# Kernel tuning notes

Hardware: AMD Instinct MI355X
Metric: run time of the kernel (lower is better)

## Reference

```python
import jax, jax.numpy as jnp
import numpy as np

B, L, T = 8, 1024, 10
K = 1.0                 # soft_sign sharpness (config.k)
S = float(np.log(9.0))  # self.s
W_PEN = 1.0             # self.w


def soft_sign(x):
    return jax.nn.sigmoid(2.0 * K * x)


def mlp2(f, W1, b1, W2, b2):
    # pointwise 2-layer MLP with ReLU after each layer; output dim 1 -> squeeze
    h = jax.nn.relu(jnp.einsum('...i,oi->...o', f, W1) + b1)
    return jax.nn.relu(jnp.einsum('...i,oi->...o', h, W2) + b2)[..., 0]


def setup_inputs() -> dict:
    key = jax.random.key(0)
    ks = jax.random.split(key, 16)
    u = jax.random.normal(ks[0], (B, L, L), jnp.float32)
    x = jax.random.uniform(ks[1], (B, L, 4), jnp.float32)
    p = lambda k, s: (jax.random.normal(k, s, jnp.float32) * 0.5)
    return dict(
        u=u, x=x, timesteps=T,
        aW1=p(ks[2], (T, 3, 3)), ab1=p(ks[3], (T, 3)), aW2=p(ks[4], (T, 1, 3)), ab2=p(ks[5], (T, 1)),
        rW1=p(ks[6], (T, 3, 3)), rb1=p(ks[7], (T, 3)), rW2=p(ks[8], (T, 1, 3)), rb2=p(ks[9], (T, 1)),
        lW1=p(ks[10], (T, 3, 2)), lb1=p(ks[11], (T, 3)), lW2=p(ks[12], (T, 1, 3)), lb2=p(ks[13], (T, 1)),
    )


def reference(u, x, timesteps, aW1, ab1, aW2, ab2, rW1, rb1, rW2, rb2, lW1, lb1, lW2, lb2):
    # constraint matrix m: sum of symmetrized outer products of base channels
    ba, bu, bc, bg = x[:, :, 0], x[:, :, 1], x[:, :, 2], x[:, :, 3]
    def sym_outer(p, q):
        o = jnp.einsum('bi,bj->bij', p, q)
        return o + o.swapaxes(-1, -2)
    m = sym_outer(ba, bu) + sym_outer(bc, bg) + sym_outer(bu, bg)

    def contact(ah):
        aa = ah * ah
        return (aa + aa.swapaxes(-1, -2)) * 0.5 * m

    uu = soft_sign(u - S) * u
    a_hat = jax.nn.sigmoid(uu) * soft_sign(uu - S)
    a = contact(a_hat)
    lmbd = W_PEN * jax.nn.relu(jnp.sum(a, -1) - 1.0)

    outs = []
    for t in range(timesteps):  # fixed unroll, distinct params per step
        grad_a = -uu * 0.5 + (lmbd * soft_sign(jnp.sum(a, -1) - 1.0))[..., None]
        grad = a_hat * m * (grad_a + grad_a.swapaxes(-1, -2))
        feats = jnp.stack([a_hat, grad, uu], -1)  # [B,L,L,3]
        ah_new = mlp2(feats, aW1[t], ab1[t], aW2[t], ab2[t])
        rho = mlp2(feats, rW1[t], rb1[t], rW2[t], rb2[t])
        ah_new = jnp.clip(jax.nn.relu(jnp.abs(ah_new) - rho), -1.0, 1.0)
        a = contact(ah_new)
        lg = jax.nn.relu(jnp.sum(a, -1) - 1.0)
        lmbd = mlp2(jnp.stack([lmbd, lg], -1), lW1[t], lb1[t], lW2[t], lb2[t])
        a_hat = ah_new
        outs.append(a)
    return jnp.stack(outs)  # [T,B,L,L] == a_t_list[1:]
```

## Files before the change

### kernel.cpp

```cpp
#include <hip/hip_runtime.h>
#include <hip/hip_bf16.h>

#define BB 8
#define LL 1024
#define TT 10
#define TILE 64
#define NTILE (LL/TILE)
#define NPAIR (NTILE*(NTILE+1)/2)
#define SPAD 65
#define S_CONST 2.1972245773362196f

typedef __hip_bfloat16 bf16;

static __device__ __forceinline__ float sigm(float v) {
    return 1.0f / (1.0f + __expf(-v));
}

static __device__ __forceinline__ unsigned short f2bf(float v) {
    bf16 h = __float2bfloat16(v);
    unsigned short b; __builtin_memcpy(&b, &h, 2); return b;
}
static __device__ __forceinline__ float lo2f(unsigned int v) {
    return __uint_as_float(v << 16);
}
static __device__ __forceinline__ float hi2f(unsigned int v) {
    return __uint_as_float(v & 0xffff0000u);
}
static __device__ __forceinline__ unsigned int pk2(float uu, float ah) {
    return (unsigned int)f2bf(uu) | ((unsigned int)f2bf(ah) << 16);
}
static __device__ __forceinline__ unsigned int pk_rt(float uu_exact, float ah) {
    return (__float_as_uint(uu_exact) >> 16) | ((unsigned int)f2bf(ah) << 16);
}

static __device__ __forceinline__ void pair_from_idx(int p, int& I, int& J) {
    int i = 0;
    while (p >= NTILE - i) { p -= NTILE - i; i++; }
    I = i; J = i + p;
}

static __device__ __forceinline__ float mlp3(float f0, float f1, float f2, const float* w) {
    float h0 = fmaxf(w[0]*f0 + w[1]*f1 + w[2]*f2 + w[9],  0.0f);
    float h1 = fmaxf(w[3]*f0 + w[4]*f1 + w[5]*f2 + w[10], 0.0f);
    float h2 = fmaxf(w[6]*f0 + w[7]*f1 + w[8]*f2 + w[11], 0.0f);
    return fmaxf(w[12]*h0 + w[13]*h1 + w[14]*h2 + w[15], 0.0f);
}

static __device__ __forceinline__ float ahnew_calc(float ah, float grad, float uuv, const float* w) {
    float va = mlp3(ah, grad, uuv, w);
    float vr = mlp3(ah, grad, uuv, w + 16);
    float v = fmaxf(fabsf(va) - vr, 0.0f);
    return fminf(v, 1.0f);
}

__global__ __launch_bounds__(256) void k_init(const float* __restrict__ u,
                                              const float* __restrict__ x,
                                              unsigned int* __restrict__ st,
                                              float* __restrict__ rs0) {
    __shared__ float stA[TILE * SPAD];
    __shared__ float stB[TILE * SPAD];
    __shared__ float xI[4 * TILE], xJ[4 * TILE];
    __shared__ float rsI[TILE], rsJ[TILE];

    int b = blockIdx.x / NPAIR, p = blockIdx.x % NPAIR;
    int I, J; pair_from_idx(p, I, J);
    int Ib = I * TILE, Jb = J * TILE;
    bool diag = (I == J);
    int tid = threadIdx.x, c = tid & 63, rg = tid >> 6;

    { int row = tid >> 2, k2 = tid & 3;
      xI[k2*TILE + row] = x[((size_t)b*LL + Ib + row)*4 + k2];
      xJ[k2*TILE + row] = x[((size_t)b*LL + Jb + row)*4 + k2]; }
    if (tid < TILE) { rsI[tid] = 0.0f; rsJ[tid] = 0.0f; }

    float ahv[16];
    size_t baseIJ = ((size_t)b*LL + Ib)*LL + Jb;
    #pragma unroll
    for (int k = 0; k < 16; k++) {
        size_t idx = baseIJ + (size_t)(rg + 4*k)*LL + c;
        float uv  = u[idx];
        float uuv = sigm(2.0f*(uv - S_CONST)) * uv;
        float ah  = sigm(uuv) * sigm(2.0f*(uuv - S_CONST));
        unsigned int pkd = pk2(uuv, ah);
        st[idx] = pkd;
        ahv[k] = hi2f(pkd);
    }
    size_t baseJI = ((size_t)b*LL + Jb)*LL + Ib;
    #pragma unroll
    for (int k = 0; k < 16; k++) {
        int xr = rg + 4*k;
        size_t idx = baseJI + (size_t)xr*LL + c;
        float uv  = u[idx];
        float uuv = sigm(2.0f*(uv - S_CONST)) * uv;
        float ah  = sigm(uuv) * sigm(2.0f*(uuv - S_CONST));
        unsigned int pkd = pk2(uuv, ah);
        if (!diag) st[idx] = pkd;
        stB[xr*SPAD + c] = hi2f(pkd);
    }
    __syncthreads();

    float buj = xJ[1*TILE + c], bgj = xJ[3*TILE + c];
    float s1j = xJ[0*TILE + c] + bgj;
    float s2j = xJ[2*TILE + c] + buj;
    float rsJ_th = 0.0f;
    #pragma unroll
    for (int k = 0; k < 16; k++) {
        int r = rg + 4*k;
        float ah_ij = ahv[k];
        float ah_ji = stB[c*SPAD + r];
        float m = xI[0*TILE + r]*buj + xI[2*TILE + r]*bgj
                + xI[1*TILE + r]*s1j + xI[3*TILE + r]*s2j;
        float a0 = 0.5f * (ah_ij*ah_ij + ah_ji*ah_ji) * m;
        stA[c*SPAD + r] = a0;
        rsJ_th += a0;
    }
    if (!diag) atomicAdd(&rsJ[c], rsJ_th);
    __syncthreads();
    { int r = tid & 63, g = tid >> 6;
      float s = 0.0f;
      #pragma unroll
      for (int q = 0; q < 16; q++) s += stA[(g*16 + q)*SPAD + r];
      atomicAdd(&rsI[r], s); }
    __syncthreads();
    if (tid < TILE) atomicAdd(&rs0[b*LL + Ib + tid], rsI[tid]);
    else if (!diag && tid < 2*TILE) atomicAdd(&rs0[b*LL + Jb + (tid - TILE)], rsJ[tid - TILE]);
}

__global__ __launch_bounds__(256) void k_step(
        unsigned int* __restrict__ st, const float* __restrict__ x,
        const float* __restrict__ rs_cur, float* __restrict__ rs_next,
        const float* __restrict__ lmbd_prev, float* __restrict__ lmbd_next,
        const float* __restrict__ aW1, const float* __restrict__ ab1,
        const float* __restrict__ aW2, const float* __restrict__ ab2,
        const float* __restrict__ rW1, const float* __restrict__ rb1,
        const float* __restrict__ rW2, const float* __restrict__ rb2,
        const float* __restrict__ lw1, const float* __restrict__ lb1_,
        const float* __restrict__ lw2, const float* __restrict__ lb2_,
        float* __restrict__ out, int t) {
    __shared__ float stA[TILE * SPAD];
    __shared__ float stB[TILE * SPAD];
    __shared__ float xI[4 * TILE], xJ[4 * TILE];
    __shared__ float lsI[TILE], lsJ[TILE];
    __shared__ float w[32];
    __shared__ float rsI[TILE], rsJ[TILE];

    int b = blockIdx.x / NPAIR, p = blockIdx.x % NPAIR;
    int I, J; pair_from_idx(p, I, J);
    int Ib = I * TILE, Jb = J * TILE;
    bool diag = (I == J);
    int tid = threadIdx.x, c = tid & 63, rg = tid >> 6;

    float uuv[16], ahv[16];
    size_t baseIJ = ((size_t)b*LL + Ib)*LL + Jb;
    #pragma unroll
    for (int k = 0; k < 16; k++) {
        unsigned int v = st[baseIJ + (size_t)(rg + 4*k)*LL + c];
        uuv[k] = lo2f(v);
        ahv[k] = hi2f(v);
    }

    if (tid < 32) {
        float v;
        if      (tid <  9) v = aW1[t*9 + tid];
        else if (tid < 12) v = ab1[t*3 + (tid-9)];
        else if (tid < 15) v = aW2[t*3 + (tid-12)];
        else if (tid < 16) v = ab2[t];
        else if (tid < 25) v = rW1[t*9 + (tid-16)];
        else if (tid < 28) v = rb1[t*3 + (tid-25)];
        else if (tid < 31) v = rW2[t*3 + (tid-28)];
        else               v = rb2[t];
        w[tid] = v;
    }
    { int row = tid >> 2, k2 = tid & 3;
      xI[k2*TILE + row] = x[((size_t)b*LL + Ib + row)*4 + k2];
      xJ[k2*TILE + row] = x[((size_t)b*LL + Jb + row)*4 + k2]; }
    if (tid < TILE) { rsI[tid] = 0.0f; rsJ[tid] = 0.0f; }
    if (tid < 128) {
        int row = (tid < 64) ? (Ib + tid) : (Jb + tid - 64);
        float rsv = rs_cur[b*LL + row];
        float lg  = fmaxf(rsv - 1.0f, 0.0f);
        float lam;
        if (t == 0) {
            lam = lg;
        } else {
            float l0 = lmbd_prev[b*LL + row];
            float h0 = fmaxf(lw1[0]*l0 + lw1[1]*lg + lb1_[0], 0.0f);
            float h1 = fmaxf(lw1[2]*l0 + lw1[3]*lg + lb1_[1], 0.0f);
            float h2 = fmaxf(lw1[4]*l0 + lw1[5]*lg + lb1_[2], 0.0f);
            lam = fmaxf(lw2[0]*h0 + lw2[1]*h1 + lw2[2]*h2 + lb2_[0], 0.0f);
        }
        float lsv = lam * sigm(2.0f*(rsv - 1.0f));
        if (tid < 64) {
            lsI[tid] = lsv;
            if (diag) lmbd_next[b*LL + row] = lam;
        } else {
            lsJ[tid - 64] = lsv;
        }
    }
    size_t baseJI = ((size_t)b*LL + Jb)*LL + Ib;
    #pragma unroll
    for (int k = 0; k < 16; k++) {
        int xr = rg + 4*k;
        unsigned int v = st[baseJI + (size_t)xr*LL + c];
        stA[xr*SPAD + c] = lo2f(v);
        stB[xr*SPAD + c] = hi2f(v);
    }
    __syncthreads();

    float buj = xJ[1*TILE + c], bgj = xJ[3*TILE + c];
    float s1j = xJ[0*TILE + c] + bgj;
    float s2j = xJ[2*TILE + c] + buj;
    size_t outBase = (((size_t)t*BB + b) * LL) * LL;
    float rsJ_th = 0.0f;
    #pragma unroll
    for (int k = 0; k < 16; k++) {
        int r = rg + 4*k;
        size_t idxIJ = baseIJ + (size_t)r*LL + c;
        float uu_ij = uuv[k];
        float ah_ij = ahv[k];
        float uu_ji = stA[c*SPAD + r];
        float ah_ji = stB[c*SPAD + r];
        float m = xI[0*TILE + r]*buj + xI[2*TILE + r]*bgj
                + xI[1*TILE + r]*s1j + xI[3*TILE + r]*s2j;
        float gsum = -0.5f * (uu_ij + uu_ji) + lsI[r] + lsJ[c];
        float an_ij = ahnew_calc(ah_ij, ah_ij * m * gsum, uu_ij, w);
        float an_ji = ahnew_calc(ah_ji, ah_ji * m * gsum, uu_ji, w);
        float a_val = 0.5f * (an_ij*an_ij + an_ji*an_ji) * m;

        st[idxIJ] = pk_rt(uu_ij, an_ij);
        __builtin_nontemporal_store(a_val, &out[outBase + (size_t)(Ib + r)*LL + (Jb + c)]);

        stA[c*SPAD + r] = a_val;
        stB[c*SPAD + r] = __uint_as_float(pk_rt(uu_ji, an_ji));
        rsJ_th += a_val;
    }
    if (!diag) atomicAdd(&rsJ[c], rsJ_th);
    __syncthreads();
    if (!diag) {
        #pragma unroll
        for (int k = 0; k < 16; k++) {
            int xr = rg + 4*k;
            st[baseJI + (size_t)xr*LL + c] = __float_as_uint(stB[xr*SPAD + c]);
            __builtin_nontemporal_store(stA[xr*SPAD + c],
                                        &out[outBase + (size_t)(Jb + xr)*LL + (Ib + c)]);
        }
    }
    if (t != TT-1) {
        int r = tid & 63, g = tid >> 6;
        float s = 0.0f;
        #pragma unroll
        for (int q = 0; q < 16; q++) s += stA[(g*16 + q)*SPAD + r];
        atomicAdd(&rsI[r], s);
        __syncthreads();
        if (tid < TILE) atomicAdd(&rs_next[b*LL + Ib + tid], rsI[tid]);
        else if (!diag && tid < 2*TILE) atomicAdd(&rs_next[b*LL + Jb + (tid - TILE)], rsJ[tid - TILE]);
    }
}

extern "C" void kernel_launch(void* const* d_in, const int* in_sizes, int n_in,
                              void* d_out, int out_size, void* d_ws, size_t ws_size,
                              hipStream_t stream) {
    const float* u   = (const float*)d_in[0];
    const float* x   = (const float*)d_in[1];
    const float* aW1 = (const float*)d_in[3];
    const float* ab1 = (const float*)d_in[4];
    const float* aW2 = (const float*)d_in[5];
    const float* ab2 = (const float*)d_in[6];
    const float* rW1 = (const float*)d_in[7];
    const float* rb1 = (const float*)d_in[8];
    const float* rW2 = (const float*)d_in[9];
    const float* rb2 = (const float*)d_in[10];
    const float* lW1 = (const float*)d_in[11];
    const float* lb1 = (const float*)d_in[12];
    const float* lW2 = (const float*)d_in[13];
    const float* lb2 = (const float*)d_in[14];
    float* out = (float*)d_out;

    char* ws = (char*)d_ws;
    size_t stBytes = (size_t)BB * LL * LL * sizeof(unsigned int);
    unsigned int* st = (unsigned int*)ws;
    float* rs    = (float*)(ws + stBytes);
    float* lmbdA = rs + (size_t)TT * BB * LL;
    float* lmbdB = lmbdA + BB * LL;

    hipMemsetAsync(rs, 0, (size_t)TT * BB * LL * sizeof(float), stream);
    hipLaunchKernelGGL(k_init, dim3(BB*NPAIR), dim3(256), 0, stream, u, x, st, rs);

    for (int t = 0; t < TT; ++t) {
        float* lnext = (t & 1) ? lmbdB : lmbdA;
        float* lprev = (t & 1) ? lmbdA : lmbdB;
        const float* rs_cur = rs + (size_t)t * BB * LL;
        float* rs_nextp = (t < TT-1) ? (rs + (size_t)(t+1) * BB * LL) : rs;
        int toff = (t > 0) ? (t - 1) : 0;
        hipLaunchKernelGGL(k_step, dim3(BB*NPAIR), dim3(256), 0, stream,
                           st, x, rs_cur, rs_nextp, lprev, lnext,
                           aW1, ab1, aW2, ab2, rW1, rb1, rW2, rb2,
                           lW1 + toff*6, lb1 + toff*3, lW2 + toff*3, lb2 + toff,
                           out, t);
    }
}
```

Measured before the change: 591.2 us.

## Fuse all timesteps into one persistent kernel with LDS-resident state and grid barriers

```diff
diff --git a/kernel.cpp b/kernel.cpp
--- a/kernel.cpp
+++ b/kernel.cpp
@@ -5,9 +5,9 @@
 #define LL 1024
 #define TT 10
 #define TILE 64
-#define NTILE (LL/TILE)
-#define NPAIR (NTILE*(NTILE+1)/2)
-#define SPAD 65
+#define NTILE 16
+#define NOFF 120
+#define NBLK 1024
 #define S_CONST 2.1972245773362196f
 
 typedef __hip_bfloat16 bf16;
@@ -15,28 +15,27 @@
 static __device__ __forceinline__ float sigm(float v) {
     return 1.0f / (1.0f + __expf(-v));
 }
-
 static __device__ __forceinline__ unsigned short f2bf(float v) {
     bf16 h = __float2bfloat16(v);
     unsigned short b; __builtin_memcpy(&b, &h, 2); return b;
 }
-static __device__ __forceinline__ float lo2f(unsigned int v) {
-    return __uint_as_float(v << 16);
-}
-static __device__ __forceinline__ float hi2f(unsigned int v) {
-    return __uint_as_float(v & 0xffff0000u);
-}
+static __device__ __forceinline__ float lo2f(unsigned int v) { return __uint_as_float(v << 16); }
+static __device__ __forceinline__ float hi2f(unsigned int v) { return __uint_as_float(v & 0xffff0000u); }
 static __device__ __forceinline__ unsigned int pk2(float uu, float ah) {
     return (unsigned int)f2bf(uu) | ((unsigned int)f2bf(ah) << 16);
 }
-static __device__ __forceinline__ unsigned int pk_rt(float uu_exact, float ah) {
-    return (__float_as_uint(uu_exact) >> 16) | ((unsigned int)f2bf(ah) << 16);
-}
-
-static __device__ __forceinline__ void pair_from_idx(int p, int& I, int& J) {
-    int i = 0;
-    while (p >= NTILE - i) { p -= NTILE - i; i++; }
-    I = i; J = i + p;
+
+static __device__ __forceinline__ void grid_bar(unsigned int* bar, int slot) {
+    __syncthreads();
+    if (threadIdx.x == 0) {
+        __hip_atomic_fetch_add(&bar[slot], 1u, __ATOMIC_ACQ_REL, __HIP_MEMORY_SCOPE_AGENT);
+        for (int it = 0; it < (1 << 21); ++it) {
+            if (__hip_atomic_load(&bar[slot], __ATOMIC_ACQUIRE, __HIP_MEMORY_SCOPE_AGENT) >= NBLK)
+                break;
+            __builtin_amdgcn_s_sleep(8);
+        }
+    }
+    __syncthreads();
 }
 
 static __device__ __forceinline__ float mlp3(float f0, float f1, float f2, const float* w) {
@@ -45,7 +44,6 @@
     float h2 = fmaxf(w[6]*f0 + w[7]*f1 + w[8]*f2 + w[11], 0.0f);
     return fmaxf(w[12]*h0 + w[13]*h1 + w[14]*h2 + w[15], 0.0f);
 }
-
 static __device__ __forceinline__ float ahnew_calc(float ah, float grad, float uuv, const float* w) {
     float va = mlp3(ah, grad, uuv, w);
     float vr = mlp3(ah, grad, uuv, w + 16);
@@ -53,207 +51,302 @@
     return fminf(v, 1.0f);
 }
 
-__global__ __launch_bounds__(256) void k_init(const float* __restrict__ u,
-                                              const float* __restrict__ x,
-                                              unsigned int* __restrict__ st,
-                                              float* __restrict__ rs0) {
-    __shared__ float stA[TILE * SPAD];
-    __shared__ float stB[TILE * SPAD];
-    __shared__ float xI[4 * TILE], xJ[4 * TILE];
-    __shared__ float rsI[TILE], rsJ[TILE];
-
-    int b = blockIdx.x / NPAIR, p = blockIdx.x % NPAIR;
-    int I, J; pair_from_idx(p, I, J);
-    int Ib = I * TILE, Jb = J * TILE;
-    bool diag = (I == J);
-    int tid = threadIdx.x, c = tid & 63, rg = tid >> 6;
-
-    { int row = tid >> 2, k2 = tid & 3;
-      xI[k2*TILE + row] = x[((size_t)b*LL + Ib + row)*4 + k2];
-      xJ[k2*TILE + row] = x[((size_t)b*LL + Jb + row)*4 + k2]; }
-    if (tid < TILE) { rsI[tid] = 0.0f; rsJ[tid] = 0.0f; }
-
-    float ahv[16];
-    size_t baseIJ = ((size_t)b*LL + Ib)*LL + Jb;
-    #pragma unroll
-    for (int k = 0; k < 16; k++) {
-        size_t idx = baseIJ + (size_t)(rg + 4*k)*LL + c;
-        float uv  = u[idx];
-        float uuv = sigm(2.0f*(uv - S_CONST)) * uv;
-        float ah  = sigm(uuv) * sigm(2.0f*(uuv - S_CONST));
-        unsigned int pkd = pk2(uuv, ah);
-        st[idx] = pkd;
-        ahv[k] = hi2f(pkd);
-    }
-    size_t baseJI = ((size_t)b*LL + Jb)*LL + Ib;
-    #pragma unroll
-    for (int k = 0; k < 16; k++) {
-        int xr = rg + 4*k;
-        size_t idx = baseJI + (size_t)xr*LL + c;
-        float uv  = u[idx];
-        float uuv = sigm(2.0f*(uv - S_CONST)) * uv;
-        float ah  = sigm(uuv) * sigm(2.0f*(uuv - S_CONST));
-        unsigned int pkd = pk2(uuv, ah);
-        if (!diag) st[idx] = pkd;
-        stB[xr*SPAD + c] = hi2f(pkd);
-    }
-    __syncthreads();
-
-    float buj = xJ[1*TILE + c], bgj = xJ[3*TILE + c];
-    float s1j = xJ[0*TILE + c] + bgj;
-    float s2j = xJ[2*TILE + c] + buj;
-    float rsJ_th = 0.0f;
-    #pragma unroll
-    for (int k = 0; k < 16; k++) {
-        int r = rg + 4*k;
-        float ah_ij = ahv[k];
-        float ah_ji = stB[c*SPAD + r];
-        float m = xI[0*TILE + r]*buj + xI[2*TILE + r]*bgj
-                + xI[1*TILE + r]*s1j + xI[3*TILE + r]*s2j;
-        float a0 = 0.5f * (ah_ij*ah_ij + ah_ji*ah_ji) * m;
-        stA[c*SPAD + r] = a0;
-        rsJ_th += a0;
-    }
-    if (!diag) atomicAdd(&rsJ[c], rsJ_th);
-    __syncthreads();
-    { int r = tid & 63, g = tid >> 6;
-      float s = 0.0f;
-      #pragma unroll
-      for (int q = 0; q < 16; q++) s += stA[(g*16 + q)*SPAD + r];
-      atomicAdd(&rsI[r], s); }
-    __syncthreads();
-    if (tid < TILE) atomicAdd(&rs0[b*LL + Ib + tid], rsI[tid]);
-    else if (!diag && tid < 2*TILE) atomicAdd(&rs0[b*LL + Jb + (tid - TILE)], rsJ[tid - TILE]);
-}
-
-__global__ __launch_bounds__(256) void k_step(
-        unsigned int* __restrict__ st, const float* __restrict__ x,
-        const float* __restrict__ rs_cur, float* __restrict__ rs_next,
-        const float* __restrict__ lmbd_prev, float* __restrict__ lmbd_next,
+__global__ __launch_bounds__(256, 4) void k_main(
+        const float* __restrict__ u, const float* __restrict__ x,
+        float* __restrict__ rs, unsigned int* __restrict__ bar,
+        float* __restrict__ out,
         const float* __restrict__ aW1, const float* __restrict__ ab1,
         const float* __restrict__ aW2, const float* __restrict__ ab2,
         const float* __restrict__ rW1, const float* __restrict__ rb1,
         const float* __restrict__ rW2, const float* __restrict__ rb2,
-        const float* __restrict__ lw1, const float* __restrict__ lb1_,
-        const float* __restrict__ lw2, const float* __restrict__ lb2_,
-        float* __restrict__ out, int t) {
-    __shared__ float stA[TILE * SPAD];
-    __shared__ float stB[TILE * SPAD];
-    __shared__ float xI[4 * TILE], xJ[4 * TILE];
+        const float* __restrict__ lW1, const float* __restrict__ lb1,
+        const float* __restrict__ lW2, const float* __restrict__ lb2) {
+    __shared__ unsigned int stA[TILE * 65];
+    __shared__ unsigned int stB[TILE * 65];
+    __shared__ float buf[8 * 65];
+    __shared__ float xIl[4 * TILE];
     __shared__ float lsI[TILE], lsJ[TILE];
+    __shared__ float rsIb[TILE], rsJb[TILE];
     __shared__ float w[32];
-    __shared__ float rsI[TILE], rsJ[TILE];
-
-    int b = blockIdx.x / NPAIR, p = blockIdx.x % NPAIR;
-    int I, J; pair_from_idx(p, I, J);
-    int Ib = I * TILE, Jb = J * TILE;
-    bool diag = (I == J);
-    int tid = threadIdx.x, c = tid & 63, rg = tid >> 6;
-
-    float uuv[16], ahv[16];
-    size_t baseIJ = ((size_t)b*LL + Ib)*LL + Jb;
-    #pragma unroll
-    for (int k = 0; k < 16; k++) {
-        unsigned int v = st[baseIJ + (size_t)(rg + 4*k)*LL + c];
-        uuv[k] = lo2f(v);
-        ahv[k] = hi2f(v);
-    }
-
-    if (tid < 32) {
-        float v;
-        if      (tid <  9) v = aW1[t*9 + tid];
-        else if (tid < 12) v = ab1[t*3 + (tid-9)];
-        else if (tid < 15) v = aW2[t*3 + (tid-12)];
-        else if (tid < 16) v = ab2[t];
-        else if (tid < 25) v = rW1[t*9 + (tid-16)];
-        else if (tid < 28) v = rb1[t*3 + (tid-25)];
-        else if (tid < 31) v = rW2[t*3 + (tid-28)];
-        else               v = rb2[t];
-        w[tid] = v;
-    }
-    { int row = tid >> 2, k2 = tid & 3;
-      xI[k2*TILE + row] = x[((size_t)b*LL + Ib + row)*4 + k2];
-      xJ[k2*TILE + row] = x[((size_t)b*LL + Jb + row)*4 + k2]; }
-    if (tid < TILE) { rsI[tid] = 0.0f; rsJ[tid] = 0.0f; }
-    if (tid < 128) {
-        int row = (tid < 64) ? (Ib + tid) : (Jb + tid - 64);
-        float rsv = rs_cur[b*LL + row];
-        float lg  = fmaxf(rsv - 1.0f, 0.0f);
-        float lam;
-        if (t == 0) {
-            lam = lg;
-        } else {
-            float l0 = lmbd_prev[b*LL + row];
-            float h0 = fmaxf(lw1[0]*l0 + lw1[1]*lg + lb1_[0], 0.0f);
-            float h1 = fmaxf(lw1[2]*l0 + lw1[3]*lg + lb1_[1], 0.0f);
-            float h2 = fmaxf(lw1[4]*l0 + lw1[5]*lg + lb1_[2], 0.0f);
-            lam = fmaxf(lw2[0]*h0 + lw2[1]*h1 + lw2[2]*h2 + lb2_[0], 0.0f);
-        }
-        float lsv = lam * sigm(2.0f*(rsv - 1.0f));
-        if (tid < 64) {
-            lsI[tid] = lsv;
-            if (diag) lmbd_next[b*LL + row] = lam;
-        } else {
-            lsJ[tid - 64] = lsv;
-        }
-    }
-    size_t baseJI = ((size_t)b*LL + Jb)*LL + Ib;
-    #pragma unroll
-    for (int k = 0; k < 16; k++) {
-        int xr = rg + 4*k;
-        unsigned int v = st[baseJI + (size_t)xr*LL + c];
-        stA[xr*SPAD + c] = lo2f(v);
-        stB[xr*SPAD + c] = hi2f(v);
-    }
-    __syncthreads();
-
-    float buj = xJ[1*TILE + c], bgj = xJ[3*TILE + c];
-    float s1j = xJ[0*TILE + c] + bgj;
-    float s2j = xJ[2*TILE + c] + buj;
-    size_t outBase = (((size_t)t*BB + b) * LL) * LL;
-    float rsJ_th = 0.0f;
-    #pragma unroll
-    for (int k = 0; k < 16; k++) {
-        int r = rg + 4*k;
-        size_t idxIJ = baseIJ + (size_t)r*LL + c;
-        float uu_ij = uuv[k];
-        float ah_ij = ahv[k];
-        float uu_ji = stA[c*SPAD + r];
-        float ah_ji = stB[c*SPAD + r];
-        float m = xI[0*TILE + r]*buj + xI[2*TILE + r]*bgj
-                + xI[1*TILE + r]*s1j + xI[3*TILE + r]*s2j;
-        float gsum = -0.5f * (uu_ij + uu_ji) + lsI[r] + lsJ[c];
-        float an_ij = ahnew_calc(ah_ij, ah_ij * m * gsum, uu_ij, w);
-        float an_ji = ahnew_calc(ah_ji, ah_ji * m * gsum, uu_ji, w);
-        float a_val = 0.5f * (an_ij*an_ij + an_ji*an_ji) * m;
-
-        st[idxIJ] = pk_rt(uu_ij, an_ij);
-        __builtin_nontemporal_store(a_val, &out[outBase + (size_t)(Ib + r)*LL + (Jb + c)]);
-
-        stA[c*SPAD + r] = a_val;
-        stB[c*SPAD + r] = __uint_as_float(pk_rt(uu_ji, an_ji));
-        rsJ_th += a_val;
-    }
-    if (!diag) atomicAdd(&rsJ[c], rsJ_th);
-    __syncthreads();
-    if (!diag) {
+
+    int gid = blockIdx.x, tid = threadIdx.x;
+    int c = tid & 63, rg = tid >> 6;
+    float lam = 0.0f;
+
+    if (gid < BB * NOFF) {
+        int b = gid / NOFF, po = gid % NOFF;
+        int i = 0; while (po >= NTILE - 1 - i) { po -= NTILE - 1 - i; i++; }
+        int Ib = i * TILE, Jb = (i + 1 + po) * TILE;
+
+        float xc0 = x[((size_t)b*LL + Jb + c)*4 + 0], xc1 = x[((size_t)b*LL + Jb + c)*4 + 1];
+        float xc2 = x[((size_t)b*LL + Jb + c)*4 + 2], xc3 = x[((size_t)b*LL + Jb + c)*4 + 3];
+        float bu_c = xc1, bg_c = xc3, s1_c = xc0 + xc3, s2_c = xc2 + xc1;
+        { int row = tid >> 2, k2 = tid & 3;
+          xIl[k2*TILE + row] = x[((size_t)b*LL + Ib + row)*4 + k2]; }
+
+        size_t ubIJ = ((size_t)b*LL + Ib)*LL + Jb;
+        size_t ubJI = ((size_t)b*LL + Jb)*LL + Ib;
         #pragma unroll
         for (int k = 0; k < 16; k++) {
-            int xr = rg + 4*k;
-            st[baseJI + (size_t)xr*LL + c] = __float_as_uint(stB[xr*SPAD + c]);
-            __builtin_nontemporal_store(stA[xr*SPAD + c],
-                                        &out[outBase + (size_t)(Jb + xr)*LL + (Ib + c)]);
-        }
-    }
-    if (t != TT-1) {
-        int r = tid & 63, g = tid >> 6;
-        float s = 0.0f;
+            int r = rg + 4*k;
+            float uv  = u[ubIJ + (size_t)r*LL + c];
+            float uuv = sigm(2.0f*(uv - S_CONST))*uv;
+            float ah  = sigm(uuv)*sigm(2.0f*(uuv - S_CONST));
+            stA[r*65 + c] = pk2(uuv, ah);
+            uv  = u[ubJI + (size_t)r*LL + c];
+            uuv = sigm(2.0f*(uv - S_CONST))*uv;
+            ah  = sigm(uuv)*sigm(2.0f*(uuv - S_CONST));
+            stB[r*65 + c] = pk2(uuv, ah);
+        }
+        if (tid < 64) rsIb[tid] = 0.0f; else if (tid < 128) rsJb[tid-64] = 0.0f;
+        __syncthreads();
+
+        {
+            float rsJacc = 0.0f;
+            for (int q = 0; q < 8; q++) {
+                #pragma unroll
+                for (int kk = 0; kk < 2; kk++) {
+                    int jj = 4*kk + rg, r = 8*q + jj;
+                    float ah_ij = hi2f(stA[r*65 + c]);
+                    float ah_ji = hi2f(stB[c*65 + r]);
+                    float m = xIl[0*TILE+r]*bu_c + xIl[2*TILE+r]*bg_c
+                            + xIl[1*TILE+r]*s1_c + xIl[3*TILE+r]*s2_c;
+                    float a0 = 0.5f*(ah_ij*ah_ij + ah_ji*ah_ji)*m;
+                    buf[jj*65 + c] = a0;
+                    rsJacc += a0;
+                }
+                __syncthreads();
+                { int jj = tid & 7, rowb = tid >> 3;
+                  float acc = buf[jj*65 + rowb] + buf[jj*65 + rowb + 32];
+                  atomicAdd(&rsIb[8*q + jj], acc); }
+                __syncthreads();
+            }
+            atomicAdd(&rsJb[c], rsJacc);
+            __syncthreads();
+            if (tid < 64) atomicAdd(&rs[b*LL + Ib + tid], rsIb[tid]);
+            else if (tid < 128) atomicAdd(&rs[b*LL + Jb + (tid-64)], rsJb[tid-64]);
+        }
+        grid_bar(bar, 0);
+
+        for (int t = 0; t < TT; t++) {
+            const float* rs_cur = rs + (size_t)t*BB*LL;
+            if (tid < 128) {
+                int row = (tid < 64) ? (Ib + tid) : (Jb + tid - 64);
+                float rsv = __hip_atomic_load(&rs_cur[b*LL + row], __ATOMIC_RELAXED, __HIP_MEMORY_SCOPE_AGENT);
+                float lg = fmaxf(rsv - 1.0f, 0.0f);
+                if (t == 0) lam = lg;
+                else {
+                    int o = t - 1;
+                    float h0 = fmaxf(lW1[o*6+0]*lam + lW1[o*6+1]*lg + lb1[o*3+0], 0.0f);
+                    float h1 = fmaxf(lW1[o*6+2]*lam + lW1[o*6+3]*lg + lb1[o*3+1], 0.0f);
+                    float h2 = fmaxf(lW1[o*6+4]*lam + lW1[o*6+5]*lg + lb1[o*3+2], 0.0f);
+                    lam = fmaxf(lW2[o*3+0]*h0 + lW2[o*3+1]*h1 + lW2[o*3+2]*h2 + lb2[o], 0.0f);
+                }
+                float lsv = lam * sigm(2.0f*(rsv - 1.0f));
+                if (tid < 64) { lsI[tid] = lsv; rsIb[tid] = 0.0f; }
+                else          { lsJ[tid-64] = lsv; rsJb[tid-64] = 0.0f; }
+            }
+            if (tid < 32) {
+                float v;
+                if      (tid <  9) v = aW1[t*9 + tid];
+                else if (tid < 12) v = ab1[t*3 + (tid-9)];
+                else if (tid < 15) v = aW2[t*3 + (tid-12)];
+                else if (tid < 16) v = ab2[t];
+                else if (tid < 25) v = rW1[t*9 + (tid-16)];
+                else if (tid < 28) v = rb1[t*3 + (tid-25)];
+                else if (tid < 31) v = rW2[t*3 + (tid-28)];
+                else               v = rb2[t];
+                w[tid] = v;
+            }
+            __syncthreads();
+
+            size_t outBase = (((size_t)t*BB + b)*LL)*LL;
+            bool last = (t == TT-1);
+            float* rs_next = rs + (size_t)(t+1)*BB*LL;
+            float rsJacc = 0.0f;
+            for (int q = 0; q < 8; q++) {
+                #pragma unroll
+                for (int kk = 0; kk < 2; kk++) {
+                    int jj = 4*kk + rg, r = 8*q + jj;
+                    unsigned int vA = stA[r*65 + c], vB = stB[c*65 + r];
+                    float uu_ij = lo2f(vA), ah_ij = hi2f(vA);
+                    float uu_ji = lo2f(vB), ah_ji = hi2f(vB);
+                    float m = xIl[0*TILE+r]*bu_c + xIl[2*TILE+r]*bg_c
+                            + xIl[1*TILE+r]*s1_c + xIl[3*TILE+r]*s2_c;
+                    float gsum = -0.5f*(uu_ij + uu_ji) + lsI[r] + lsJ[c];
+                    float an_ij = ahnew_calc(ah_ij, ah_ij*m*gsum, uu_ij, w);
+                    float an_ji = ahnew_calc(ah_ji, ah_ji*m*gsum, uu_ji, w);
+                    float a_val = 0.5f*(an_ij*an_ij + an_ji*an_ji)*m;
+                    ((unsigned short*)stA)[(r*65 + c)*2 + 1] = f2bf(an_ij);
+                    ((unsigned short*)stB)[(c*65 + r)*2 + 1] = f2bf(an_ji);
+                    __builtin_nontemporal_store(a_val, &out[outBase + (size_t)(Ib+r)*LL + (Jb+c)]);
+                    buf[jj*65 + c] = a_val;
+                    rsJacc += a_val;
+                }
+                __syncthreads();
+                { int jj = tid & 7, rowb = tid >> 3;
+                  float acc = 0.0f;
+                  #pragma unroll
+                  for (int s = 0; s < 2; s++) {
+                      int row = rowb + 32*s;
+                      float v = buf[jj*65 + row];
+                      __builtin_nontemporal_store(v, &out[outBase + (size_t)(Jb+row)*LL + (Ib + 8*q + jj)]);
+                      acc += v;
+                  }
+                  if (!last) atomicAdd(&rsIb[8*q + jj], acc); }
+                __syncthreads();
+            }
+            if (!last) {
+                atomicAdd(&rsJb[c], rsJacc);
+                __syncthreads();
+                if (tid < 64) atomicAdd(&rs_next[b*LL + Ib + tid], rsIb[tid]);
+                else if (tid < 128) atomicAdd(&rs_next[b*LL + Jb + (tid-64)], rsJb[tid-64]);
+                grid_bar(bar, 1 + t);
+            }
+        }
+    } else {
+        int d = gid - BB*NOFF;
+        int g0 = 2*d;
+        int b = g0 >> 4;
+        int Ab = (g0 & 15) * TILE, Bb = ((g0 & 15) + 1) * TILE;
+        float* xIlB = buf;
+
+        float t0, t1, t2, t3;
+        t0 = x[((size_t)b*LL + Ab + c)*4 + 0]; t1 = x[((size_t)b*LL + Ab + c)*4 + 1];
+        t2 = x[((size_t)b*LL + Ab + c)*4 + 2]; t3 = x[((size_t)b*LL + Ab + c)*4 + 3];
+        float buA = t1, bgA = t3, s1A = t0 + t3, s2A = t2 + t1;
+        t0 = x[((size_t)b*LL + Bb + c)*4 + 0]; t1 = x[((size_t)b*LL + Bb + c)*4 + 1];
+        t2 = x[((size_t)b*LL + Bb + c)*4 + 2]; t3 = x[((size_t)b*LL + Bb + c)*4 + 3];
+        float buB = t1, bgB = t3, s1B = t0 + t3, s2B = t2 + t1;
+        { int row = tid >> 2, k2 = tid & 3;
+          xIl [k2*TILE + row] = x[((size_t)b*LL + Ab + row)*4 + k2];
+          xIlB[k2*TILE + row] = x[((size_t)b*LL + Bb + row)*4 + k2]; }
+
+        size_t ubA = ((size_t)b*LL + Ab)*LL + Ab;
+        size_t ubB = ((size_t)b*LL + Bb)*LL + Bb;
         #pragma unroll
-        for (int q = 0; q < 16; q++) s += stA[(g*16 + q)*SPAD + r];
-        atomicAdd(&rsI[r], s);
+        for (int k = 0; k < 16; k++) {
+            int r = rg + 4*k;
+            float uv  = u[ubA + (size_t)r*LL + c];
+            float uuv = sigm(2.0f*(uv - S_CONST))*uv;
+            float ah  = sigm(uuv)*sigm(2.0f*(uuv - S_CONST));
+            stA[r*65 + c] = pk2(uuv, ah);
+            uv  = u[ubB + (size_t)r*LL + c];
+            uuv = sigm(2.0f*(uv - S_CONST))*uv;
+            ah  = sigm(uuv)*sigm(2.0f*(uuv - S_CONST));
+            stB[r*65 + c] = pk2(uuv, ah);
+        }
+        if (tid < 64) rsIb[tid] = 0.0f; else if (tid < 128) rsJb[tid-64] = 0.0f;
         __syncthreads();
-        if (tid < TILE) atomicAdd(&rs_next[b*LL + Ib + tid], rsI[tid]);
-        else if (!diag && tid < 2*TILE) atomicAdd(&rs_next[b*LL + Jb + (tid - TILE)], rsJ[tid - TILE]);
+        {
+            float accA = 0.0f, accB = 0.0f;
+            #pragma unroll
+            for (int k = 0; k < 16; k++) {
+                int r = rg + 4*k;
+                float aij = hi2f(stA[r*65 + c]), aji = hi2f(stA[c*65 + r]);
+                float m = xIl[0*TILE+r]*buA + xIl[2*TILE+r]*bgA
+                        + xIl[1*TILE+r]*s1A + xIl[3*TILE+r]*s2A;
+                accA += 0.5f*(aij*aij + aji*aji)*m;
+                aij = hi2f(stB[r*65 + c]); aji = hi2f(stB[c*65 + r]);
+                m = xIlB[0*TILE+r]*buB + xIlB[2*TILE+r]*bgB
+                  + xIlB[1*TILE+r]*s1B + xIlB[3*TILE+r]*s2B;
+                accB += 0.5f*(aij*aij + aji*aji)*m;
+            }
+            atomicAdd(&rsIb[c], accA);
+            atomicAdd(&rsJb[c], accB);
+            __syncthreads();
+            if (tid < 64) atomicAdd(&rs[b*LL + Ab + tid], rsIb[tid]);
+            else if (tid < 128) atomicAdd(&rs[b*LL + Bb + (tid-64)], rsJb[tid-64]);
+        }
+        grid_bar(bar, 0);
+
+        for (int t = 0; t < TT; t++) {
+            const float* rs_cur = rs + (size_t)t*BB*LL;
+            if (tid < 128) {
+                int row = (tid < 64) ? (Ab + tid) : (Bb + tid - 64);
+                float rsv = __hip_atomic_load(&rs_cur[b*LL + row], __ATOMIC_RELAXED, __HIP_MEMORY_SCOPE_AGENT);
+                float lg = fmaxf(rsv - 1.0f, 0.0f);
+                if (t == 0) lam = lg;
+                else {
+                    int o = t - 1;
+                    float h0 = fmaxf(lW1[o*6+0]*lam + lW1[o*6+1]*lg + lb1[o*3+0], 0.0f);
+                    float h1 = fmaxf(lW1[o*6+2]*lam + lW1[o*6+3]*lg + lb1[o*3+1], 0.0f);
+                    float h2 = fmaxf(lW1[o*6+4]*lam + lW1[o*6+5]*lg + lb1[o*3+2], 0.0f);
+                    lam = fmaxf(lW2[o*3+0]*h0 + lW2[o*3+1]*h1 + lW2[o*3+2]*h2 + lb2[o], 0.0f);
+                }
+                float lsv = lam * sigm(2.0f*(rsv - 1.0f));
+                if (tid < 64) { lsI[tid] = lsv; rsIb[tid] = 0.0f; }
+                else          { lsJ[tid-64] = lsv; rsJb[tid-64] = 0.0f; }
+            }
+            if (tid < 32) {
+                float v;
+                if      (tid <  9) v = aW1[t*9 + tid];
+                else if (tid < 12) v = ab1[t*3 + (tid-9)];
+                else if (tid < 15) v = aW2[t*3 + (tid-12)];
+                else if (tid < 16) v = ab2[t];
+                else if (tid < 25) v = rW1[t*9 + (tid-16)];
+                else if (tid < 28) v = rb1[t*3 + (tid-25)];
+                else if (tid < 31) v = rW2[t*3 + (tid-28)];
+                else               v = rb2[t];
+                w[tid] = v;
+            }
+            __syncthreads();
+
+            size_t outBase = (((size_t)t*BB + b)*LL)*LL;
+            bool last = (t == TT-1);
+            float* rs_next = rs + (size_t)(t+1)*BB*LL;
+
+            unsigned int vT[16];
+            #pragma unroll
+            for (int k = 0; k < 16; k++) vT[k] = stA[c*65 + (rg + 4*k)];
+            __syncthreads();
+            float acc = 0.0f;
+            #pragma unroll
+            for (int k = 0; k < 16; k++) {
+                int r = rg + 4*k;
+                unsigned int vO = stA[r*65 + c];
+                float uu_ij = lo2f(vO), ah_ij = hi2f(vO);
+                float uu_ji = lo2f(vT[k]), ah_ji = hi2f(vT[k]);
+                float m = xIl[0*TILE+r]*buA + xIl[2*TILE+r]*bgA
+                        + xIl[1*TILE+r]*s1A + xIl[3*TILE+r]*s2A;
+                float gsum = -0.5f*(uu_ij + uu_ji) + lsI[r] + lsI[c];
+                float an_ij = ahnew_calc(ah_ij, ah_ij*m*gsum, uu_ij, w);
+                float an_ji = ahnew_calc(ah_ji, ah_ji*m*gsum, uu_ji, w);
+                float a_val = 0.5f*(an_ij*an_ij + an_ji*an_ji)*m;
+                ((unsigned short*)stA)[(r*65 + c)*2 + 1] = f2bf(an_ij);
+                __builtin_nontemporal_store(a_val, &out[outBase + (size_t)(Ab+r)*LL + (Ab+c)]);
+                acc += a_val;
+            }
+            if (!last) atomicAdd(&rsIb[c], acc);
+
+            #pragma unroll
+            for (int k = 0; k < 16; k++) vT[k] = stB[c*65 + (rg + 4*k)];
+            __syncthreads();
+            acc = 0.0f;
+            #pragma unroll
+            for (int k = 0; k < 16; k++) {
+                int r = rg + 4*k;
+                unsigned int vO = stB[r*65 + c];
+                float uu_ij = lo2f(vO), ah_ij = hi2f(vO);
+                float uu_ji = lo2f(vT[k]), ah_ji = hi2f(vT[k]);
+                float m = xIlB[0*TILE+r]*buB + xIlB[2*TILE+r]*bgB
+                        + xIlB[1*TILE+r]*s1B + xIlB[3*TILE+r]*s2B;
+                float gsum = -0.5f*(uu_ij + uu_ji) + lsJ[r] + lsJ[c];
+                float an_ij = ahnew_calc(ah_ij, ah_ij*m*gsum, uu_ij, w);
+                float an_ji = ahnew_calc(ah_ji, ah_ji*m*gsum, uu_ji, w);
+                float a_val = 0.5f*(an_ij*an_ij + an_ji*an_ji)*m;
+                ((unsigned short*)stB)[(r*65 + c)*2 + 1] = f2bf(an_ij);
+                __builtin_nontemporal_store(a_val, &out[outBase + (size_t)(Bb+r)*LL + (Bb+c)]);
+                acc += a_val;
+            }
+            if (!last) {
+                atomicAdd(&rsJb[c], acc);
+                __syncthreads();
+                if (tid < 64) atomicAdd(&rs_next[b*LL + Ab + tid], rsIb[tid]);
+                else if (tid < 128) atomicAdd(&rs_next[b*LL + Bb + (tid-64)], rsJb[tid-64]);
+                grid_bar(bar, 1 + t);
+            }
+        }
     }
 }
 
@@ -276,26 +369,12 @@
     const float* lb2 = (const float*)d_in[14];
     float* out = (float*)d_out;
 
-    char* ws = (char*)d_ws;
-    size_t stBytes = (size_t)BB * LL * LL * sizeof(unsigned int);
-    unsigned int* st = (unsigned int*)ws;
-    float* rs    = (float*)(ws + stBytes);
-    float* lmbdA = rs + (size_t)TT * BB * LL;
-    float* lmbdB = lmbdA + BB * LL;
-
-    hipMemsetAsync(rs, 0, (size_t)TT * BB * LL * sizeof(float), stream);
-    hipLaunchKernelGGL(k_init, dim3(BB*NPAIR), dim3(256), 0, stream, u, x, st, rs);
-
-    for (int t = 0; t < TT; ++t) {
-        float* lnext = (t & 1) ? lmbdB : lmbdA;
-        float* lprev = (t & 1) ? lmbdA : lmbdB;
-        const float* rs_cur = rs + (size_t)t * BB * LL;
-        float* rs_nextp = (t < TT-1) ? (rs + (size_t)(t+1) * BB * LL) : rs;
-        int toff = (t > 0) ? (t - 1) : 0;
-        hipLaunchKernelGGL(k_step, dim3(BB*NPAIR), dim3(256), 0, stream,
-                           st, x, rs_cur, rs_nextp, lprev, lnext,
-                           aW1, ab1, aW2, ab2, rW1, rb1, rW2, rb2,
-                           lW1 + toff*6, lb1 + toff*3, lW2 + toff*3, lb2 + toff,
-                           out, t);
-    }
-}
+    float* rs = (float*)d_ws;
+    unsigned int* bar = (unsigned int*)(rs + (size_t)TT * BB * LL);
+    hipMemsetAsync(rs, 0, (size_t)TT * BB * LL * sizeof(float) + 16 * sizeof(unsigned int), stream);
+
+    hipLaunchKernelGGL(k_main, dim3(NBLK), dim3(256), 0, stream,
+                       u, x, rs, bar, out,
+                       aW1, ab1, aW2, ab2, rW1, rb1, rW2, rb2,
+                       lW1, lb1, lW2, lb2);
+}
```

Measured after the change: 1.795 ms. 3.04x slower.
